# Performance work log

Hardware: AMD Instinct MI355X
Metric: run time of the kernel (lower is better)

## Reference

```python
import jax, jax.numpy as jnp
import numpy as np

N = 6144          # nodes
K = 32            # fixed out-degree -> num_nearest (static; torch derives it from max adj row sum)
L = 6             # n_layers
D = 128           # hidden_dim
M = 64            # hidden_egnn_dim (m_dim)
HE = 256          # hidden_edge_dim
NF = 68           # n_features = pos_embed_dim + 4
EMB = 128         # embedding_size


def setup_inputs() -> dict:
    key = jax.random.key(0)
    ks = iter(jax.random.split(key, 64))
    nxt = lambda: next(ks)

    def w(shape, std=0.001):  # EGNN init_: Linear weights ~ N(0, init_eps)
        return (jax.random.normal(nxt(), shape, jnp.float32) * std)

    def b(shape, fan_in):     # torch Linear default bias: U(-1/sqrt(fan_in), 1/sqrt(fan_in))
        lim = 1.0 / np.sqrt(fan_in)
        return jax.random.uniform(nxt(), shape, jnp.float32, -lim, lim)

    x = jax.random.normal(nxt(), (N, NF), jnp.float32)
    coords = jax.random.normal(nxt(), (N, 3), jnp.float32) * 10.0
    # structured edge_index: node i -> (i+1..i+K) mod N, so every row degree == K (num_nearest = K)
    src = jnp.repeat(jnp.arange(N, dtype=jnp.int32), K)
    dst = ((src + jnp.tile(jnp.arange(1, K + 1, dtype=jnp.int32), N)) % N).astype(jnp.int32)
    edge_index = jnp.stack([src, dst], axis=0)

    EIN = 2 * D + 1  # edge_mlp input dim = 257
    return {
        "x": x, "coords": coords, "edge_index": edge_index,
        "w_enc": w((NF, D)), "b_enc": b((D,), NF),
        "ew1": w((L, EIN, HE)), "eb1": b((L, HE), EIN),
        "ew2": w((L, HE, M)),  "eb2": b((L, M), HE),
        "nw1": w((L, D + M, 2 * D)), "nb1": b((L, 2 * D), D + M),
        "nw2": w((L, 2 * D, D)),     "nb2": b((L, D), 2 * D),
        "dw1": w((D, D)), "db1": b((D,), D), "dw2": w((D, D)), "db2": b((D,), D),
        "gw1": w((D, D)), "gb1": b((D,), D), "gw2": w((D, EMB)), "gb2": b((EMB,), D),
    }


def reference(x, coords, edge_index, w_enc, b_enc, ew1, eb1, ew2, eb2,
              nw1, nb1, nw2, nb2, dw1, db1, dw2, db2, gw1, gb1, gw2, gb2):
    silu = jax.nn.silu
    n = x.shape[0]

    # dense adjacency from edge list (torch sparse_coo -> to_dense().bool()), self edges removed
    adj = jnp.zeros((n, n), bool).at[edge_index[0], edge_index[1]].set(True)
    eye = jnp.eye(n, dtype=bool)
    adj = adj & ~eye

    feats = x @ w_enc + b_enc  # [n, D]

    # coords/mask never change across layers -> compute neighbor structure once (faithful hoist).
    # mask is all-True in Model.forward, so the rank_mask fill (100000.0) is a no-op.
    rel = coords[:, None, :] - coords[None, :, :]        # [n, n, 3]
    rel_dist = (rel * rel).sum(-1)                       # [n, n]
    ranking = jnp.where(eye, -1.0, jnp.where(adj, 0.0, rel_dist))
    neg_top, idx = jax.lax.top_k(-ranking, K)            # K smallest
    nbhd_mask = (-neg_top) <= 0.0                        # valid_radius = 0: keep self + adj only
    rd_sel = jnp.take_along_axis(rel_dist, idx, axis=1)[..., None]  # [n, K, 1]

    for l in range(L):
        fj = feats[idx]                                   # [n, K, D] gather
        fi = jnp.broadcast_to(feats[:, None, :], fj.shape)
        e = jnp.concatenate([fi, fj, rd_sel], axis=-1)    # [n, K, 2D+1]
        m_ij = silu(silu(e @ ew1[l] + eb1[l]) @ ew2[l] + eb2[l])
        m_ij = jnp.where(nbhd_mask[..., None], m_ij, 0.0)
        m_i = m_ij.sum(axis=-2)                           # [n, M]
        h = jnp.concatenate([feats, m_i], axis=-1)
        feats = silu(h @ nw1[l] + nb1[l]) @ nw2[l] + nb2[l] + feats

    feats = silu(feats @ dw1 + db1) @ dw2 + db2           # node_dec
    g = feats.sum(axis=0, keepdims=True)                  # scatter-sum, single graph -> [1, D]
    out = silu(g @ gw1 + gb1) @ gw2 + gb2                 # graph_dec -> [1, EMB]
    return out / jnp.maximum(jnp.linalg.norm(out, axis=1, keepdims=True), 1e-12)
```

## Files before the change

### kernel.cpp

```cpp
#include <hip/hip_runtime.h>
#include <hip/hip_bf16.h>
#include <math.h>


#define NN   6144
#define KNN  32
#define NL   6
#define DD   128
#define MM   64
#define HEE  256

typedef short bf16x8 __attribute__((ext_vector_type(8)));
typedef float f32x4  __attribute__((ext_vector_type(4)));

__device__ __forceinline__ float silu_f(float x) {
    return x / (1.0f + expf(-x));
}
__device__ __forceinline__ float silu_fast(float x) {
    return __fdividef(x, 1.0f + __expf(-x));
}
__device__ __forceinline__ unsigned short f2bf(float x) {
    __hip_bfloat16 b = __float2bfloat16(x);
    return *reinterpret_cast<unsigned short*>(&b);
}
__device__ __forceinline__ unsigned pack_bf2(float lo, float hi) {
    __hip_bfloat162 v = __float22bfloat162_rn(make_float2(lo, hi));
    return *reinterpret_cast<unsigned*>(&v);
}

template<int KN, int AW, bool SILU, bool RESID, bool PQB>
__global__ __launch_bounds__(256)
void mfma_gemm(const float* __restrict__ A, const unsigned short* __restrict__ Bp,
               const float* __restrict__ bias, float* __restrict__ C, int Nn)
{
    constexpr int NKS = KN / 32;
    constexpr int LDA = KN + 8;
    constexpr int C4  = KN / 4;
    __shared__ unsigned short lsA[64 * LDA];
    const int t = threadIdx.x;
    const int row0 = blockIdx.y * 64, col0 = blockIdx.x * 64;

#pragma unroll
    for (int u0 = 0; u0 < 64 * C4; u0 += 256) {
        int u = u0 + t;
        int r = u / C4, c4 = u % C4;
        float4 v = make_float4(0.f, 0.f, 0.f, 0.f);
        if (c4 * 4 < AW) v = *(const float4*)&A[(size_t)(row0 + r) * AW + c4 * 4];
        *(uint2*)&lsA[r * LDA + c4 * 4] = make_uint2(pack_bf2(v.x, v.y), pack_bf2(v.z, v.w));
    }
    __syncthreads();

    const int w = t >> 6, l = t & 63;
    const int wr = w & 1, wc = w >> 1;
    const int lr = l & 15, lg = l >> 4;
    const int ct0 = blockIdx.x * 4 + wc * 2;
    const int aoff = (wr * 32 + lr) * LDA + lg * 8;
    f32x4 acc[2][2] = {};
#pragma unroll
    for (int ks = 0; ks < NKS; ++ks) {
        bf16x8 a0 = *(const bf16x8*)&lsA[aoff + ks * 32];
        bf16x8 a1 = *(const bf16x8*)&lsA[aoff + 16 * LDA + ks * 32];
        bf16x8 b0 = *(const bf16x8*)&Bp[((size_t)(ct0 * NKS + ks) * 64 + l) * 8];
        bf16x8 b1 = *(const bf16x8*)&Bp[((size_t)((ct0 + 1) * NKS + ks) * 64 + l) * 8];
        acc[0][0] = __builtin_amdgcn_mfma_f32_16x16x32_bf16(a0, b0, acc[0][0], 0, 0, 0);
        acc[0][1] = __builtin_amdgcn_mfma_f32_16x16x32_bf16(a0, b1, acc[0][1], 0, 0, 0);
        acc[1][0] = __builtin_amdgcn_mfma_f32_16x16x32_bf16(a1, b0, acc[1][0], 0, 0, 0);
        acc[1][1] = __builtin_amdgcn_mfma_f32_16x16x32_bf16(a1, b1, acc[1][1], 0, 0, 0);
    }
#pragma unroll
    for (int rt = 0; rt < 2; ++rt) {
#pragma unroll
        for (int ctl = 0; ctl < 2; ++ctl) {
            int col = col0 + wc * 32 + ctl * 16 + lr;
            float bv = (!PQB || col < 256) ? bias[col] : 0.0f;
#pragma unroll
            for (int r = 0; r < 4; ++r) {
                int row = row0 + wr * 32 + rt * 16 + lg * 4 + r;
                float v = acc[rt][ctl][r] + bv;
                if (SILU) v = silu_f(v);
                size_t off = (size_t)row * Nn + col;
                if (RESID) v += C[off];
                C[off] = v;
            }
        }
    }
}

__global__ __launch_bounds__(256)
void pack_all(const float* __restrict__ ew1, const float* __restrict__ ew2,
              const float* __restrict__ nw1, const float* __restrict__ nw2,
              const float* __restrict__ dw1, const float* __restrict__ dw2,
              const float* __restrict__ wenc,
              unsigned short* __restrict__ Bpq, unsigned short* __restrict__ Bn1,
              unsigned short* __restrict__ Bn2, unsigned short* __restrict__ w2p,
              unsigned short* __restrict__ Bd1, unsigned short* __restrict__ Bd2,
              unsigned short* __restrict__ Benc)
{
    const int t = threadIdx.x;
    const int u = blockIdx.x * 4 + (t >> 6);
    if (u >= 2008) return;
    const int lane = t & 63;
    const float* src; unsigned short* dst;
    int nks, nc, ctd, ctc, ks, kmax = 1 << 30;
    if (u < 1920) {
        int l = u / 320, r = u % 320;
        if (r < 128) {
            ctd = r >> 2; ks = r & 3; nks = 4; nc = 256; ctc = ctd & 15;
            src = ew1 + (size_t)l * 257 * 256 + (ctd >= 16 ? 128 * 256 : 0);
            dst = Bpq + (size_t)l * 65536;
        } else if (r < 224) {
            int rr = r - 128; ctd = rr / 6; ks = rr % 6; nks = 6; nc = 256; ctc = ctd;
            src = nw1 + (size_t)l * 192 * 256; dst = Bn1 + (size_t)l * 49152;
        } else if (r < 288) {
            int rr = r - 224; ctd = rr >> 3; ks = rr & 7; nks = 8; nc = 128; ctc = ctd;
            src = nw2 + (size_t)l * 256 * 128; dst = Bn2 + (size_t)l * 32768;
        } else {
            int rr = r - 288; ctd = rr >> 3; ks = rr & 7; nks = 8; nc = 64; ctc = ctd;
            src = ew2 + (size_t)l * 256 * 64; dst = w2p + (size_t)l * 16384;
        }
    } else if (u < 1984) {
        int rr = u - 1920;
        int m = rr >> 5; rr &= 31;
        ctd = rr >> 2; ks = rr & 3; nks = 4; nc = 128; ctc = ctd;
        src = m ? dw2 : dw1; dst = m ? Bd2 : Bd1;
    } else {
        int rr = u - 1984;
        ctd = rr / 3; ks = rr % 3; nks = 3; nc = 128; ctc = ctd; kmax = 68;
        src = wenc; dst = Benc;
    }
    const int k0 = ks * 32 + (lane >> 4) * 8;
    const int col = ctc * 16 + (lane & 15);
    unsigned short* o = dst + ((size_t)(ctd * nks + ks) * 64 + lane) * 8;
#pragma unroll
    for (int j = 0; j < 8; ++j)
        o[j] = (k0 + j < kmax) ? f2bf(src[(size_t)(k0 + j) * nc + col]) : (unsigned short)0;
}

__global__ __launch_bounds__(256)
void neighbor_kernel(const int* __restrict__ ei, const float* __restrict__ coords,
                     int* __restrict__ idx, float* __restrict__ rd)
{
    const int gid = blockIdx.x * 256 + threadIdx.x;
    const int i = gid >> 5, k = gid & 31;
    const int j = ei[(size_t)NN * KNN + (size_t)i * KNN + k];
    int dmax = j, kmax = k;
#pragma unroll
    for (int m = 1; m < 32; m <<= 1) {
        int od = __shfl_xor(dmax, m);
        int ok = __shfl_xor(kmax, m);
        if (od > dmax) { dmax = od; kmax = ok; }
    }
    int pos, jw;
    if (k == kmax) { pos = 0; jw = i; }
    else { pos = (k < kmax) ? k + 1 : k; jw = j; }
    float dx = coords[3 * i]     - coords[3 * jw];
    float dy = coords[3 * i + 1] - coords[3 * jw + 1];
    float dz = coords[3 * i + 2] - coords[3 * jw + 2];
    rd[(size_t)i * KNN + pos]  = dx * dx + dy * dy + dz * dz;
    idx[(size_t)i * KNN + pos] = jw;
}

__global__ __launch_bounds__(256)
void edge_kernel(const float* __restrict__ PQ, const float* __restrict__ wr,
                 const unsigned short* __restrict__ w2p, const float* __restrict__ eb2,
                 const int* __restrict__ idx, const float* __restrict__ rd,
                 const float* __restrict__ feats, float* __restrict__ h)
{
    __shared__ unsigned short lsH[32 * 264];
    __shared__ float lsPart[2][4][16];
    __shared__ int   lsIdx[KNN];
    __shared__ float lsRd[KNN];

    const int i = blockIdx.x;
    const int t = threadIdx.x;

    if (t < KNN) { lsIdx[t] = idx[(size_t)i * KNN + t]; lsRd[t] = rd[(size_t)i * KNN + t]; }
    __syncthreads();

    {
        const int c0 = (t & 63) * 4;
        const int rg = t >> 6;
        float4 p4 = *(const float4*)&PQ[(size_t)i * 512 + c0];
        float4 w4 = *(const float4*)&wr[c0];
        int   jj[8]; float rr[8];
#pragma unroll
        for (int k = 0; k < 8; ++k) { jj[k] = lsIdx[rg * 8 + k]; rr[k] = lsRd[rg * 8 + k]; }
        float4 q[8];
#pragma unroll
        for (int k = 0; k < 8; ++k)
            q[k] = *(const float4*)&PQ[(size_t)jj[k] * 512 + 256 + c0];
#pragma unroll
        for (int k = 0; k < 8; ++k) {
            float a0 = silu_fast(fmaf(rr[k], w4.x, p4.x) + q[k].x);
            float a1 = silu_fast(fmaf(rr[k], w4.y, p4.y) + q[k].y);
            float a2 = silu_fast(fmaf(rr[k], w4.z, p4.z) + q[k].z);
            float a3 = silu_fast(fmaf(rr[k], w4.w, p4.w) + q[k].w);
            *(uint2*)&lsH[(rg * 8 + k) * 264 + c0] =
                make_uint2(pack_bf2(a0, a1), pack_bf2(a2, a3));
        }
    }
    __syncthreads();

    const int w = t >> 6, l = t & 63;
    const int rt = w & 1, cb = (w >> 1) * 2;
    const int lr = l & 15, lg = l >> 4;
    const int arow = rt * 16 + lr;
    f32x4 acc0 = {0.f, 0.f, 0.f, 0.f}, acc1 = {0.f, 0.f, 0.f, 0.f};
#pragma unroll
    for (int ks = 0; ks < 8; ++ks) {
        bf16x8 a  = *(const bf16x8*)&lsH[arow * 264 + ks * 32 + lg * 8];
        bf16x8 b0 = *(const bf16x8*)&w2p[(size_t)(cb * 8 + ks) * 512 + l * 8];
        bf16x8 b1 = *(const bf16x8*)&w2p[(size_t)((cb + 1) * 8 + ks) * 512 + l * 8];
        acc0 = __builtin_amdgcn_mfma_f32_16x16x32_bf16(a, b0, acc0, 0, 0, 0);
        acc1 = __builtin_amdgcn_mfma_f32_16x16x32_bf16(a, b1, acc1, 0, 0, 0);
    }
    float e0 = eb2[cb * 16 + lr], e1 = eb2[(cb + 1) * 16 + lr];
    float s0 = 0.f, s1 = 0.f;
#pragma unroll
    for (int r = 0; r < 4; ++r) {
        s0 += silu_fast(acc0[r] + e0);
        s1 += silu_fast(acc1[r] + e1);
    }
    s0 += __shfl_xor(s0, 16); s0 += __shfl_xor(s0, 32);
    s1 += __shfl_xor(s1, 16); s1 += __shfl_xor(s1, 32);
    if (lg == 0) { lsPart[rt][cb][lr] = s0; lsPart[rt][cb + 1][lr] = s1; }
    __syncthreads();

    if (t < MM) {
        float m = lsPart[0][t >> 4][t & 15] + lsPart[1][t >> 4][t & 15];
        h[(size_t)i * 192 + DD + t] = m;
    } else if (t < 192) {
        h[(size_t)i * 192 + (t - 64)] = feats[(size_t)i * DD + (t - 64)];
    }
}

__global__ __launch_bounds__(256)
void colsum_kernel(const float* __restrict__ F, float* __restrict__ partial)
{
    __shared__ float ls[2][DD];
    const int b = blockIdx.x;
    const int t = threadIdx.x;
    const int c = t & 127, rg = t >> 7;
    float s = 0.0f;
    const int r0 = b * 64;
    for (int r = rg; r < 64; r += 2) s += F[(size_t)(r0 + r) * DD + c];
    ls[rg][c] = s;
    __syncthreads();
    if (t < DD) partial[(size_t)b * DD + t] = ls[0][t] + ls[1][t];
}

__global__ __launch_bounds__(128)
void final_kernel(const float* __restrict__ partial, const float* __restrict__ gw1,
                  const float* __restrict__ gb1, const float* __restrict__ gw2,
                  const float* __restrict__ gb2, float* __restrict__ out)
{
    __shared__ float lg[DD], lu[DD], red[DD];
    const int t = threadIdx.x;
    float s = 0.0f;
    for (int b = 0; b < 96; ++b) s += partial[(size_t)b * DD + t];
    lg[t] = s;
    __syncthreads();
    float a = 0.0f;
    for (int c = 0; c < DD; ++c) a += lg[c] * gw1[(size_t)c * DD + t];
    lu[t] = silu_f(a + gb1[t]);
    __syncthreads();
    float v = 0.0f;
    for (int c = 0; c < DD; ++c) v += lu[c] * gw2[(size_t)c * DD + t];
    v += gb2[t];
    red[t] = v * v;
    __syncthreads();
    for (int sft = 64; sft > 0; sft >>= 1) {
        if (t < sft) red[t] += red[t + sft];
        __syncthreads();
    }
    float nrm = sqrtf(red[0]);
    out[t] = v / fmaxf(nrm, 1e-12f);
}

extern "C" void kernel_launch(void* const* d_in, const int* in_sizes, int n_in,
                              void* d_out, int out_size, void* d_ws, size_t ws_size,
                              hipStream_t stream)
{
    const float* x      = (const float*)d_in[0];
    const float* coords = (const float*)d_in[1];
    const int*   ei     = (const int*)d_in[2];
    const float* w_enc  = (const float*)d_in[3];
    const float* b_enc  = (const float*)d_in[4];
    const float* ew1    = (const float*)d_in[5];
    const float* eb1    = (const float*)d_in[6];
    const float* ew2    = (const float*)d_in[7];
    const float* eb2    = (const float*)d_in[8];
    const float* nw1    = (const float*)d_in[9];
    const float* nb1    = (const float*)d_in[10];
    const float* nw2    = (const float*)d_in[11];
    const float* nb2    = (const float*)d_in[12];
    const float* dw1    = (const float*)d_in[13];
    const float* db1    = (const float*)d_in[14];
    const float* dw2    = (const float*)d_in[15];
    const float* db2    = (const float*)d_in[16];
    const float* gw1    = (const float*)d_in[17];
    const float* gb1    = (const float*)d_in[18];
    const float* gw2    = (const float*)d_in[19];
    const float* gb2    = (const float*)d_in[20];
    float* out = (float*)d_out;

    float* ws      = (float*)d_ws;
    float* feats   = ws;
    float* PQ      = feats + 786432;
    float* hbuf    = PQ + 3145728;
    int*   idxbuf  = (int*)(hbuf + 1179648);
    float* rdbuf   = (float*)(idxbuf + 196608);
    float* partial = rdbuf + 196608;
    unsigned short* w2p  = (unsigned short*)(partial + 12288);
    unsigned short* Bpq  = w2p + 98304;
    unsigned short* Bn1  = Bpq + 393216;
    unsigned short* Bn2  = Bn1 + 294912;
    unsigned short* Bd1  = Bn2 + 196608;
    unsigned short* Bd2  = Bd1 + 16384;
    unsigned short* Benc = Bd2 + 16384;

    float* Tbuf = PQ;
    float* Ubuf = PQ;
    float* Fbuf = PQ + 786432;

    dim3 blk(256);

    neighbor_kernel<<<768, blk, 0, stream>>>(ei, coords, idxbuf, rdbuf);
    pack_all<<<502, blk, 0, stream>>>(ew1, ew2, nw1, nw2, dw1, dw2, w_enc,
                                      Bpq, Bn1, Bn2, w2p, Bd1, Bd2, Benc);
    mfma_gemm<96, 68, false, false, false><<<dim3(2, 96), blk, 0, stream>>>(
        x, Benc, b_enc, feats, 128);

    for (int l = 0; l < NL; ++l) {
        const float* W1 = ew1 + (size_t)l * 257 * 256;
        mfma_gemm<128, 128, false, false, true><<<dim3(8, 96), blk, 0, stream>>>(
            feats, Bpq + (size_t)l * 65536, eb1 + l * 256, PQ, 512);
        edge_kernel<<<NN, blk, 0, stream>>>(PQ, W1 + 256 * 256, w2p + (size_t)l * 16384,
                                            eb2 + l * 64, idxbuf, rdbuf, feats, hbuf);
        mfma_gemm<192, 192, true, false, false><<<dim3(4, 96), blk, 0, stream>>>(
            hbuf, Bn1 + (size_t)l * 49152, nb1 + l * 256, Tbuf, 256);
        mfma_gemm<256, 256, false, true, false><<<dim3(2, 96), blk, 0, stream>>>(
            Tbuf, Bn2 + (size_t)l * 32768, nb2 + l * 128, feats, 128);
    }

    mfma_gemm<128, 128, true, false, false><<<dim3(2, 96), blk, 0, stream>>>(feats, Bd1, db1, Ubuf, 128);
    mfma_gemm<128, 128, false, false, false><<<dim3(2, 96), blk, 0, stream>>>(Ubuf, Bd2, db2, Fbuf, 128);
    colsum_kernel<<<96, blk, 0, stream>>>(Fbuf, partial);
    final_kernel<<<1, dim3(128), 0, stream>>>(partial, gw1, gb1, gw2, gb2, out);
}
```

Before: 522.1 us.

## Fuse node MLP, residual and next-layer PQ projection into one kernel

Adds a node_mlp kernel that runs both node-MLP GEMMs, the residual add, and the next layer's per-node edge projection (PQ) for a 32-row tile, keeping intermediates in LDS as bf16. The edge kernel now writes only the aggregated messages instead of copying feats into a concatenated buffer, and the node decoder's two GEMMs are fused the same way. This removes several launches per layer and the global round trips for the hidden activations. Each block does more serial work with only 192 blocks, which may leave the GPU under-occupied. A sched_barrier is also added in the edge kernel so the gather loads are kept together.

```diff
diff --git a/kernel.cpp b/kernel.cpp
--- a/kernel.cpp
+++ b/kernel.cpp
@@ -81,6 +81,132 @@
                 size_t off = (size_t)row * Nn + col;
                 if (RESID) v += C[off];
                 C[off] = v;
+            }
+        }
+    }
+}
+
+template<int KA, int KH, bool RESID, bool PQOUT>
+__global__ __launch_bounds__(256, 4)
+void node_mlp(const float* __restrict__ feats, const float* __restrict__ mbuf,
+              const unsigned short* __restrict__ B1, const float* __restrict__ b1,
+              const unsigned short* __restrict__ B2, const float* __restrict__ b2,
+              const unsigned short* __restrict__ Bpq, const float* __restrict__ eb1,
+              float* __restrict__ outF, float* __restrict__ PQ)
+{
+    constexpr int LDA = KA + 8;
+    constexpr int LDT = KH + 8;
+    constexpr int KS1 = KA / 32;
+    constexpr int KS2 = KH / 32;
+    constexpr int CT1 = KH / 64;
+    constexpr int C4A = KA / 4;
+    __shared__ unsigned short lsA[32 * LDA];
+    __shared__ unsigned short lsT[32 * LDT];
+    __shared__ unsigned short lsF[PQOUT ? 32 * 136 : 4];
+    const int t = threadIdx.x;
+    const int r0 = blockIdx.x * 32;
+
+#pragma unroll
+    for (int u0 = 0; u0 < 32 * C4A; u0 += 256) {
+        int u = u0 + t;
+        int r = u / C4A, c = (u % C4A) * 4;
+        float4 v;
+        if (KA == 128 || c < 128) v = *(const float4*)&feats[(size_t)(r0 + r) * DD + c];
+        else                      v = *(const float4*)&mbuf[(size_t)(r0 + r) * MM + (c - 128)];
+        *(uint2*)&lsA[r * LDA + c] = make_uint2(pack_bf2(v.x, v.y), pack_bf2(v.z, v.w));
+    }
+    __syncthreads();
+
+    const int w = t >> 6, l = t & 63;
+    const int lr = l & 15, lg = l >> 4;
+
+    {
+        f32x4 acc[2][CT1] = {};
+#pragma unroll
+        for (int ks = 0; ks < KS1; ++ks) {
+            bf16x8 a0 = *(const bf16x8*)&lsA[lr * LDA + ks * 32 + lg * 8];
+            bf16x8 a1 = *(const bf16x8*)&lsA[(16 + lr) * LDA + ks * 32 + lg * 8];
+#pragma unroll
+            for (int ct = 0; ct < CT1; ++ct) {
+                bf16x8 b = *(const bf16x8*)&B1[((size_t)((w * CT1 + ct) * KS1 + ks) * 64 + l) * 8];
+                acc[0][ct] = __builtin_amdgcn_mfma_f32_16x16x32_bf16(a0, b, acc[0][ct], 0, 0, 0);
+                acc[1][ct] = __builtin_amdgcn_mfma_f32_16x16x32_bf16(a1, b, acc[1][ct], 0, 0, 0);
+            }
+        }
+#pragma unroll
+        for (int rt = 0; rt < 2; ++rt)
+#pragma unroll
+        for (int ct = 0; ct < CT1; ++ct) {
+            int col = (w * CT1 + ct) * 16 + lr;
+            float bv = b1[col];
+#pragma unroll
+            for (int r = 0; r < 4; ++r) {
+                int row = rt * 16 + lg * 4 + r;
+                lsT[row * LDT + col] = f2bf(silu_f(acc[rt][ct][r] + bv));
+            }
+        }
+    }
+    __syncthreads();
+
+    {
+        f32x4 acc[2][2] = {};
+#pragma unroll
+        for (int ks = 0; ks < KS2; ++ks) {
+            bf16x8 a0 = *(const bf16x8*)&lsT[lr * LDT + ks * 32 + lg * 8];
+            bf16x8 a1 = *(const bf16x8*)&lsT[(16 + lr) * LDT + ks * 32 + lg * 8];
+#pragma unroll
+            for (int ct = 0; ct < 2; ++ct) {
+                bf16x8 b = *(const bf16x8*)&B2[((size_t)((w * 2 + ct) * KS2 + ks) * 64 + l) * 8];
+                acc[0][ct] = __builtin_amdgcn_mfma_f32_16x16x32_bf16(a0, b, acc[0][ct], 0, 0, 0);
+                acc[1][ct] = __builtin_amdgcn_mfma_f32_16x16x32_bf16(a1, b, acc[1][ct], 0, 0, 0);
+            }
+        }
+#pragma unroll
+        for (int rt = 0; rt < 2; ++rt)
+#pragma unroll
+        for (int ct = 0; ct < 2; ++ct) {
+            int col = (w * 2 + ct) * 16 + lr;
+            float bv = b2[col];
+#pragma unroll
+            for (int r = 0; r < 4; ++r) {
+                int row = rt * 16 + lg * 4 + r;
+                size_t off = (size_t)(r0 + row) * DD + col;
+                float v = acc[rt][ct][r] + bv;
+                if (RESID) v += feats[off];
+                outF[off] = v;
+                if (PQOUT) lsF[row * 136 + col] = f2bf(v);
+            }
+        }
+    }
+
+    if (PQOUT) {
+        __syncthreads();
+#pragma unroll
+        for (int cp = 0; cp < 2; ++cp) {
+            f32x4 acc[2][4] = {};
+#pragma unroll
+            for (int ks = 0; ks < 4; ++ks) {
+                bf16x8 a0 = *(const bf16x8*)&lsF[lr * 136 + ks * 32 + lg * 8];
+                bf16x8 a1 = *(const bf16x8*)&lsF[(16 + lr) * 136 + ks * 32 + lg * 8];
+#pragma unroll
+                for (int ct = 0; ct < 4; ++ct) {
+                    int ctg = w * 8 + cp * 4 + ct;
+                    bf16x8 b = *(const bf16x8*)&Bpq[((size_t)(ctg * 4 + ks) * 64 + l) * 8];
+                    acc[0][ct] = __builtin_amdgcn_mfma_f32_16x16x32_bf16(a0, b, acc[0][ct], 0, 0, 0);
+                    acc[1][ct] = __builtin_amdgcn_mfma_f32_16x16x32_bf16(a1, b, acc[1][ct], 0, 0, 0);
+                }
+            }
+#pragma unroll
+            for (int rt = 0; rt < 2; ++rt)
+#pragma unroll
+            for (int ct = 0; ct < 4; ++ct) {
+                int col = (w * 8 + cp * 4 + ct) * 16 + lr;
+                float bv = (col < 256) ? eb1[col] : 0.0f;
+#pragma unroll
+                for (int r = 0; r < 4; ++r) {
+                    int row = rt * 16 + lg * 4 + r;
+                    PQ[(size_t)(r0 + row) * 512 + col] = acc[rt][ct][r] + bv;
+                }
             }
         }
     }
@@ -164,7 +290,7 @@
 void edge_kernel(const float* __restrict__ PQ, const float* __restrict__ wr,
                  const unsigned short* __restrict__ w2p, const float* __restrict__ eb2,
                  const int* __restrict__ idx, const float* __restrict__ rd,
-                 const float* __restrict__ feats, float* __restrict__ h)
+                 float* __restrict__ mbuf)
 {
     __shared__ unsigned short lsH[32 * 264];
     __shared__ float lsPart[2][4][16];
@@ -189,6 +315,7 @@
 #pragma unroll
         for (int k = 0; k < 8; ++k)
             q[k] = *(const float4*)&PQ[(size_t)jj[k] * 512 + 256 + c0];
+        __builtin_amdgcn_sched_barrier(0);
 #pragma unroll
         for (int k = 0; k < 8; ++k) {
             float a0 = silu_fast(fmaf(rr[k], w4.x, p4.x) + q[k].x);
@@ -226,12 +353,8 @@
     if (lg == 0) { lsPart[rt][cb][lr] = s0; lsPart[rt][cb + 1][lr] = s1; }
     __syncthreads();
 
-    if (t < MM) {
-        float m = lsPart[0][t >> 4][t & 15] + lsPart[1][t >> 4][t & 15];
-        h[(size_t)i * 192 + DD + t] = m;
-    } else if (t < 192) {
-        h[(size_t)i * 192 + (t - 64)] = feats[(size_t)i * DD + (t - 64)];
-    }
+    if (t < MM)
+        mbuf[(size_t)i * MM + t] = lsPart[0][t >> 4][t & 15] + lsPart[1][t >> 4][t & 15];
 }
 
 __global__ __launch_bounds__(256)
@@ -307,8 +430,8 @@
     float* ws      = (float*)d_ws;
     float* feats   = ws;
     float* PQ      = feats + 786432;
-    float* hbuf    = PQ + 3145728;
-    int*   idxbuf  = (int*)(hbuf + 1179648);
+    float* mbuf    = PQ + 3145728;
+    int*   idxbuf  = (int*)(mbuf + 393216);
     float* rdbuf   = (float*)(idxbuf + 196608);
     float* partial = rdbuf + 196608;
     unsigned short* w2p  = (unsigned short*)(partial + 12288);
@@ -319,9 +442,7 @@
     unsigned short* Bd2  = Bd1 + 16384;
     unsigned short* Benc = Bd2 + 16384;
 
-    float* Tbuf = PQ;
-    float* Ubuf = PQ;
-    float* Fbuf = PQ + 786432;
+    float* Fbuf = PQ;
 
     dim3 blk(256);
 
@@ -330,21 +451,28 @@
                                       Bpq, Bn1, Bn2, w2p, Bd1, Bd2, Benc);
     mfma_gemm<96, 68, false, false, false><<<dim3(2, 96), blk, 0, stream>>>(
         x, Benc, b_enc, feats, 128);
+    mfma_gemm<128, 128, false, false, true><<<dim3(8, 96), blk, 0, stream>>>(
+        feats, Bpq, eb1, PQ, 512);
 
     for (int l = 0; l < NL; ++l) {
         const float* W1 = ew1 + (size_t)l * 257 * 256;
-        mfma_gemm<128, 128, false, false, true><<<dim3(8, 96), blk, 0, stream>>>(
-            feats, Bpq + (size_t)l * 65536, eb1 + l * 256, PQ, 512);
         edge_kernel<<<NN, blk, 0, stream>>>(PQ, W1 + 256 * 256, w2p + (size_t)l * 16384,
-                                            eb2 + l * 64, idxbuf, rdbuf, feats, hbuf);
-        mfma_gemm<192, 192, true, false, false><<<dim3(4, 96), blk, 0, stream>>>(
-            hbuf, Bn1 + (size_t)l * 49152, nb1 + l * 256, Tbuf, 256);
-        mfma_gemm<256, 256, false, true, false><<<dim3(2, 96), blk, 0, stream>>>(
-            Tbuf, Bn2 + (size_t)l * 32768, nb2 + l * 128, feats, 128);
-    }
-
-    mfma_gemm<128, 128, true, false, false><<<dim3(2, 96), blk, 0, stream>>>(feats, Bd1, db1, Ubuf, 128);
-    mfma_gemm<128, 128, false, false, false><<<dim3(2, 96), blk, 0, stream>>>(Ubuf, Bd2, db2, Fbuf, 128);
+                                            eb2 + l * 64, idxbuf, rdbuf, mbuf);
+        if (l < NL - 1) {
+            node_mlp<192, 256, true, true><<<192, blk, 0, stream>>>(
+                feats, mbuf, Bn1 + (size_t)l * 49152, nb1 + l * 256,
+                Bn2 + (size_t)l * 32768, nb2 + l * 128,
+                Bpq + (size_t)(l + 1) * 65536, eb1 + (l + 1) * 256, feats, PQ);
+        } else {
+            node_mlp<192, 256, true, false><<<192, blk, 0, stream>>>(
+                feats, mbuf, Bn1 + (size_t)l * 49152, nb1 + l * 256,
+                Bn2 + (size_t)l * 32768, nb2 + l * 128,
+                nullptr, nullptr, feats, nullptr);
+        }
+    }
+
+    node_mlp<128, 128, false, false><<<192, blk, 0, stream>>>(
+        feats, nullptr, Bd1, db1, Bd2, db2, nullptr, nullptr, Fbuf, nullptr);
     colsum_kernel<<<96, blk, 0, stream>>>(Fbuf, partial);
     final_kernel<<<1, dim3(128), 0, stream>>>(partial, gw1, gb1, gw2, gb2, out);
 }
```

After: 464.7 us. 1.12x faster.
